# Performance work log

Hardware: AMD Instinct MI355X
Metric: run time of the kernel (lower is better)

Reference implementation:

```python
import jax, jax.numpy as jnp
import numpy as np

HID = 128
HEADS = 4
CH = HID // HEADS          # 32
EDGE_DIM = 2 * HID         # H_update mode
GROUPS = 8
NEG_SLOPE = 0.2
EPS_GN = 1e-5
EPS_LN = 1e-5
N_NODES = 32768
N_EDGES = 524288


def setup_inputs() -> dict:
    key = jax.random.key(0)
    ks = jax.random.split(key, 32)
    N, E, C = N_NODES, N_EDGES, HID
    s = lambda fan: 1.0 / np.sqrt(fan)
    inp = dict(
        h_target=jax.random.normal(ks[0], (N, C), jnp.float32),
        h_source=jax.random.normal(ks[1], (N, C), jnp.float32),
        pos=jax.random.normal(ks[2], (N, 2), jnp.float32),
        t_emb=jax.random.normal(ks[3], (N, C), jnp.float32),
        edge_index=jax.random.randint(ks[4], (2, E), 0, N, jnp.int32),
        # AdaGN params
        gn_gamma=jnp.ones((C,), jnp.float32),
        gn_beta=jnp.zeros((C,), jnp.float32),
        fc_W=jax.random.normal(ks[5], (C, 2 * C), jnp.float32) * s(C),
        fc_b=jnp.zeros((2 * C,), jnp.float32),
        # GATv2 params
        Wl=jax.random.normal(ks[6], (C, HEADS * CH), jnp.float32) * s(C),
        bl=jnp.zeros((HEADS * CH,), jnp.float32),
        Wr=jax.random.normal(ks[7], (C, HEADS * CH), jnp.float32) * s(C),
        br=jnp.zeros((HEADS * CH,), jnp.float32),
        We=jax.random.normal(ks[8], (EDGE_DIM, HEADS * CH), jnp.float32) * s(EDGE_DIM),
        att=jax.random.normal(ks[9], (HEADS, CH), jnp.float32) * s(CH),
        gat_bias=jnp.zeros((HEADS * CH,), jnp.float32),
        # post GAT linear
        Wpost=jax.random.normal(ks[10], (C, C), jnp.float32) * s(C),
        bpost=jnp.zeros((C,), jnp.float32),
        # update MLP: LayerNorm -> Linear -> GELU -> Linear
        ln_g=jnp.ones((C,), jnp.float32),
        ln_b=jnp.zeros((C,), jnp.float32),
        W1=jax.random.normal(ks[11], (C, C), jnp.float32) * s(C),
        b1=jnp.zeros((C,), jnp.float32),
        W2=jax.random.normal(ks[12], (C, C), jnp.float32) * s(C),
        b2=jnp.zeros((C,), jnp.float32),
    )
    return inp


def _adagn(x, cond, gn_gamma, gn_beta, fc_W, fc_b):
    N, C = x.shape
    xg = x.reshape(N, GROUPS, C // GROUPS)
    mu = xg.mean(-1, keepdims=True)
    var = xg.var(-1, keepdims=True)
    normed = ((xg - mu) * jax.lax.rsqrt(var + EPS_GN)).reshape(N, C)
    normed = normed * gn_gamma + gn_beta
    style = cond @ fc_W + fc_b
    gamma, beta = jnp.split(style, 2, axis=-1)
    return normed * (1.0 + gamma) + beta


def reference(h_target, h_source, pos, t_emb, edge_index,
              gn_gamma, gn_beta, fc_W, fc_b,
              Wl, bl, Wr, br, We, att, gat_bias,
              Wpost, bpost, ln_g, ln_b, W1, b1, W2, b2):
    N, C = h_source.shape
    src, dst = edge_index[0], edge_index[1]

    h_src_mod = _adagn(h_source, t_emb, gn_gamma, gn_beta, fc_W, fc_b)

    # physics edge features (H_update mode)
    d_vec = pos[src] - pos[dst]                       # [E,2]
    dx, dy = d_vec[:, 0:1], d_vec[:, 1:2]
    dist_sq = jnp.maximum((d_vec ** 2).sum(-1, keepdims=True), 1e-8)
    grad_mag = (h_src_mod[src] - h_src_mod[dst]) / dist_sq   # [E,C]
    edge_attr = jnp.concatenate([grad_mag * (-dy), grad_mag * dx], axis=-1)  # [E,2C]

    # GATv2Conv (eval mode, no dropout)
    xl = (h_src_mod @ Wl + bl).reshape(N, HEADS, CH)  # source transform
    xr = (h_src_mod @ Wr + br).reshape(N, HEADS, CH)  # target transform
    e = (edge_attr @ We).reshape(-1, HEADS, CH)
    z = jax.nn.leaky_relu(xl[src] + xr[dst] + e, NEG_SLOPE)   # [E,H,Ch]
    logit = jnp.einsum('ehc,hc->eh', z, att)                  # [E,H]
    m = jax.ops.segment_max(logit, dst, num_segments=N)       # [N,H]
    m = jnp.where(jnp.isfinite(m), m, 0.0)
    ex = jnp.exp(logit - m[dst])
    denom = jax.ops.segment_sum(ex, dst, num_segments=N)      # [N,H]
    alpha = ex / (denom[dst] + 1e-16)                         # [E,H]
    msg = xl[src] * alpha[..., None]                          # [E,H,Ch]
    aggr = jax.ops.segment_sum(msg, dst, num_segments=N).reshape(N, HEADS * CH)
    aggr = aggr + gat_bias

    aggr = aggr @ Wpost + bpost

    # update MLP with residual
    mu = aggr.mean(-1, keepdims=True)
    var = aggr.var(-1, keepdims=True)
    ln = (aggr - mu) * jax.lax.rsqrt(var + EPS_LN) * ln_g + ln_b
    h = jax.nn.gelu(ln @ W1 + b1, approximate=False) @ W2 + b2
    return h_target + h
```

## Files before the change

### kernel.cpp

```cpp
#include <hip/hip_runtime.h>
#include <hip/hip_bf16.h>
#include <math.h>

#define HID 128

typedef __bf16 bf16x8 __attribute__((ext_vector_type(8)));
typedef float f32x4 __attribute__((ext_vector_type(4)));
typedef float nf4 __attribute__((ext_vector_type(4)));
union BF8 { uint4 u; bf16x8 v; unsigned short s[8]; };

__device__ __forceinline__ unsigned short f2bf(float x) {
  unsigned u = __float_as_uint(x);
  unsigned r = u + 0x7FFFu + ((u >> 16) & 1u);
  return (unsigned short)(r >> 16);
}
__device__ __forceinline__ float bf2f(unsigned short h) {
  return __uint_as_float(((unsigned)h) << 16);
}
__device__ __forceinline__ void ld2bf(const unsigned short* p, float& x, float& y) {
  unsigned v = *(const unsigned*)p;
  x = __uint_as_float((v & 0xFFFFu) << 16);
  y = __uint_as_float(v & 0xFFFF0000u);
}
__device__ __forceinline__ float2 pk_add2(float2 a, float2 b) {
  return make_float2(a.x + b.x, a.y + b.y);
}
__device__ __forceinline__ float2 pk_sub2(float2 a, float2 b) {
  return make_float2(a.x - b.x, a.y - b.y);
}
__device__ __forceinline__ float2 pk_fma2(float2 a, float2 b, float2 c) {
  return make_float2(fmaf(a.x, b.x, c.x), fmaf(a.y, b.y, c.y));
}
__device__ __forceinline__ float2 pk_max2(float2 a, float2 b) {
  return make_float2(fmaxf(a.x, b.x), fmaxf(a.y, b.y));
}
__device__ __forceinline__ float2 pk_muls2(float2 a, float b) {
  return make_float2(a.x * b, a.y * b);
}

__global__ __launch_bounds__(256) void k1_prep_hist(
    const float* __restrict__ fc_W, const float* __restrict__ Wl,
    const float* __restrict__ Wr, const float* __restrict__ We,
    const float* __restrict__ Wpost, const float* __restrict__ W1,
    const float* __restrict__ W2, const float* __restrict__ bl,
    const float* __restrict__ br, const float* __restrict__ gat_bias,
    const float* __restrict__ bpost,
    unsigned short* __restrict__ fcTh, unsigned short* __restrict__ fcTl,
    unsigned short* __restrict__ WnTh, unsigned short* __restrict__ WnTl,
    unsigned short* __restrict__ WpT, unsigned short* __restrict__ W1T,
    unsigned short* __restrict__ W2T,
    float* __restrict__ bxy, float* __restrict__ bpost2,
    const int* __restrict__ edst, int* __restrict__ count, int E) {
  int bid = blockIdx.x;
  if (bid >= 578) {
    int e = (bid - 578) * 256 + threadIdx.x;
    if (e < E) atomicAdd(&count[edst[e]], 1);
    return;
  }
  int gid = bid * 256 + threadIdx.x;
  if (gid < 32768) {
    int n = gid >> 7, k = gid & 127;
    float x = fc_W[k * 256 + n];
    unsigned short h = f2bf(x);
    fcTh[n * 128 + k] = h;
    fcTl[n * 128 + k] = f2bf(x - bf2f(h));
  } else if (gid < 98304) {
    int i = gid - 32768; int n = i >> 7, k = i & 127;
    float x;
    if (n < 128)      x = Wl[k * 128 + n];
    else if (n < 256) x = Wr[k * 128 + (n - 128)];
    else if (n < 384) x = We[k * 128 + (n - 256)];
    else              x = We[(128 + k) * 128 + (n - 384)];
    unsigned short h = f2bf(x);
    WnTh[n * 128 + k] = h;
    if (n >= 256) WnTl[(n - 256) * 128 + k] = f2bf(x - bf2f(h));
  } else if (gid < 147456) {
    int i = gid - 98304; int which = i >> 14; int j = i & 16383;
    int n = j >> 7, k = j & 127;
    const float* W = (which == 0) ? Wpost : (which == 1) ? W1 : W2;
    unsigned short* T = (which == 0) ? WpT : (which == 1) ? W1T : W2T;
    T[n * 128 + k] = f2bf(W[k * 128 + n]);
  } else if (gid < 147712) {
    int j = gid - 147456;
    bxy[j] = (j < 128) ? bl[j] : br[j - 128];
  } else if (gid < 147840) {
    int t = gid - 147712;
    float s = bpost[t];
    for (int k = 0; k < 128; ++k) s += gat_bias[k] * Wpost[k * 128 + t];
    bpost2[t] = s;
  }
}

__global__ __launch_bounds__(256) void k2_style_scan(
    const float* __restrict__ A, const unsigned short* __restrict__ WTh,
    const unsigned short* __restrict__ WTl, const float* __restrict__ bias,
    float* __restrict__ C,
    const int* __restrict__ count, int* __restrict__ rowptr,
    int* __restrict__ cursor, int N, int E) {
  if (blockIdx.x == 512) {
    __shared__ int wtot[4];
    int t = threadIdx.x, lane = t & 63, wv = t >> 6;
    const int4* c4 = (const int4*)count;
    int base = t * 32;
    int s = 0;
    for (int i = 0; i < 32; ++i) {
      int4 c = c4[base + i];
      s += c.x + c.y + c.z + c.w;
    }
    int incl = s;
#pragma unroll
    for (int off = 1; off < 64; off <<= 1) {
      int v = __shfl_up(incl, off);
      if (lane >= off) incl += v;
    }
    if (lane == 63) wtot[wv] = incl;
    __syncthreads();
    if (t == 0) {
      int a0 = wtot[0], a1 = wtot[1], a2 = wtot[2];
      wtot[0] = 0; wtot[1] = a0; wtot[2] = a0 + a1; wtot[3] = a0 + a1 + a2;
    }
    __syncthreads();
    int run = wtot[wv] + incl - s;
    for (int i = 0; i < 32; ++i) {
      int4 c = c4[base + i];
      int4 r;
      r.x = run; run += c.x;
      r.y = run; run += c.y;
      r.z = run; run += c.z;
      r.w = run; run += c.w;
      ((int4*)rowptr)[base + i] = r;
      ((int4*)cursor)[base + i] = r;
    }
    if (t == 255) rowptr[N] = E;
    return;
  }
  int tid = threadIdx.x;
  int wave = tid >> 6, lane = tid & 63;
  int m = lane & 15, q = lane >> 4;
  int r0 = blockIdx.x * 64 + wave * 16;
  const float* arow = A + (size_t)(r0 + m) * 128 + q * 8;
  BF8 Ah[4], Al[4];
#pragma unroll
  for (int kc = 0; kc < 4; ++kc) {
    float4 x0 = *(const float4*)(arow + kc * 32);
    float4 x1 = *(const float4*)(arow + kc * 32 + 4);
    float xs[8] = {x0.x, x0.y, x0.z, x0.w, x1.x, x1.y, x1.z, x1.w};
#pragma unroll
    for (int j = 0; j < 8; ++j) {
      unsigned short h = f2bf(xs[j]);
      Ah[kc].s[j] = h;
      Al[kc].s[j] = f2bf(xs[j] - bf2f(h));
    }
  }
  for (int nt = 0; nt < 16; ++nt) {
    const unsigned short* wr  = WTh + (size_t)(nt * 16 + m) * 128 + q * 8;
    const unsigned short* wrl = WTl + (size_t)(nt * 16 + m) * 128 + q * 8;
    f32x4 acc = {0.f, 0.f, 0.f, 0.f};
#pragma unroll
    for (int kc = 0; kc < 4; ++kc) {
      BF8 bh, blo;
      bh.u  = *(const uint4*)(wr + kc * 32);
      blo.u = *(const uint4*)(wrl + kc * 32);
      acc = __builtin_amdgcn_mfma_f32_16x16x32_bf16(Ah[kc].v, bh.v, acc, 0, 0, 0);
      acc = __builtin_amdgcn_mfma_f32_16x16x32_bf16(Al[kc].v, bh.v, acc, 0, 0, 0);
      acc = __builtin_amdgcn_mfma_f32_16x16x32_bf16(Ah[kc].v, blo.v, acc, 0, 0, 0);
    }
    int n = nt * 16 + m;
    float bv = bias[n];
#pragma unroll
    for (int i = 0; i < 4; ++i) {
      int row = r0 + q * 4 + i;
      C[(size_t)row * 256 + n] = acc[i] + bv;
    }
  }
}

__global__ __launch_bounds__(256) void k3_node_scatter(
    const float* __restrict__ h_source, const float* __restrict__ style,
    const float* __restrict__ gn_gamma, const float* __restrict__ gn_beta,
    const unsigned short* __restrict__ WnTh, const unsigned short* __restrict__ WnTl,
    const float* __restrict__ bxy,
    unsigned short* __restrict__ packed, unsigned short* __restrict__ xrArr,
    const int* __restrict__ esrc, const int* __restrict__ edst,
    const float* __restrict__ pos, int* __restrict__ cursor,
    nf4* __restrict__ meta, int E) {
  int bid = blockIdx.x;
  if (bid >= 256) {
    int e = (bid - 256) * 256 + threadIdx.x;
    if (e >= E) return;
    int src = esrc[e], dst = edst[e];
    int p = atomicAdd(&cursor[dst], 1);
    float2 ps = *(const float2*)(pos + 2 * src);
    float2 pd = *(const float2*)(pos + 2 * dst);
    float dx = ps.x - pd.x, dy = ps.y - pd.y;
    float d2 = fmaxf(dx * dx + dy * dy, 1e-8f);
    nf4 v = {__int_as_float(src), -dy / d2, dx / d2, 0.0f};
    meta[p] = v;
    return;
  }
  int tid = threadIdx.x, wave = tid >> 6, lane = tid & 63;
  int m = lane & 15, q = lane >> 4;
  int r0 = bid * 128 + wave * 32;
  BF8 Ah[2][4], Al[2][4];
#pragma unroll
  for (int set = 0; set < 2; ++set) {
    int r = r0 + set * 16 + m;
    const float* hrow = h_source + (size_t)r * 128;
    const float* srow = style + (size_t)r * 256;
#pragma unroll
    for (int kc = 0; kc < 4; ++kc) {
      int ch = q * 8 + kc * 32;
      float4 x0 = *(const float4*)(hrow + ch);
      float4 x1 = *(const float4*)(hrow + ch + 4);
      float xs[8] = {x0.x, x0.y, x0.z, x0.w, x1.x, x1.y, x1.z, x1.w};
      float s8 = 0.f, q8 = 0.f;
#pragma unroll
      for (int j = 0; j < 8; ++j) { s8 += xs[j]; q8 += xs[j] * xs[j]; }
      float s16 = s8 + __shfl_xor(s8, 16);
      float q16 = q8 + __shfl_xor(q8, 16);
      float mu = s16 * (1.0f / 16.0f);
      float var = q16 * (1.0f / 16.0f) - mu * mu;
      float rv = rsqrtf(var + 1e-5f);
      float4 g0 = *(const float4*)(gn_gamma + ch);
      float4 g1 = *(const float4*)(gn_gamma + ch + 4);
      float4 be0 = *(const float4*)(gn_beta + ch);
      float4 be1 = *(const float4*)(gn_beta + ch + 4);
      float4 sg0 = *(const float4*)(srow + ch);
      float4 sg1 = *(const float4*)(srow + ch + 4);
      float4 sb0 = *(const float4*)(srow + 128 + ch);
      float4 sb1 = *(const float4*)(srow + 128 + ch + 4);
      float gg[8] = {g0.x, g0.y, g0.z, g0.w, g1.x, g1.y, g1.z, g1.w};
      float bb[8] = {be0.x, be0.y, be0.z, be0.w, be1.x, be1.y, be1.z, be1.w};
      float sg[8] = {sg0.x, sg0.y, sg0.z, sg0.w, sg1.x, sg1.y, sg1.z, sg1.w};
      float sb[8] = {sb0.x, sb0.y, sb0.z, sb0.w, sb1.x, sb1.y, sb1.z, sb1.w};
#pragma unroll
      for (int j = 0; j < 8; ++j) {
        float v = ((xs[j] - mu) * rv * gg[j] + bb[j]) * (1.0f + sg[j]) + sb[j];
        unsigned short h = f2bf(v);
        Ah[set][kc].s[j] = h;
        Al[set][kc].s[j] = f2bf(v - bf2f(h));
      }
    }
  }
  for (int nt = 0; nt < 32; ++nt) {
    f32x4 acc0 = {0.f, 0.f, 0.f, 0.f};
    f32x4 acc1 = {0.f, 0.f, 0.f, 0.f};
    const unsigned short* wr = WnTh + (size_t)(nt * 16 + m) * 128 + q * 8;
    if (nt < 16) {
#pragma unroll
      for (int kc = 0; kc < 4; ++kc) {
        BF8 bh; bh.u = *(const uint4*)(wr + kc * 32);
        acc0 = __builtin_amdgcn_mfma_f32_16x16x32_bf16(Ah[0][kc].v, bh.v, acc0, 0, 0, 0);
        acc1 = __builtin_amdgcn_mfma_f32_16x16x32_bf16(Ah[1][kc].v, bh.v, acc1, 0, 0, 0);
      }
    } else {
      const unsigned short* wl = WnTl + (size_t)((nt - 16) * 16 + m) * 128 + q * 8;
#pragma unroll
      for (int kc = 0; kc < 4; ++kc) {
        BF8 bh, blo;
        bh.u  = *(const uint4*)(wr + kc * 32);
        blo.u = *(const uint4*)(wl + kc * 32);
        acc0 = __builtin_amdgcn_mfma_f32_16x16x32_bf16(Ah[0][kc].v, bh.v, acc0, 0, 0, 0);
        acc0 = __builtin_amdgcn_mfma_f32_16x16x32_bf16(Al[0][kc].v, bh.v, acc0, 0, 0, 0);
        acc0 = __builtin_amdgcn_mfma_f32_16x16x32_bf16(Ah[0][kc].v, blo.v, acc0, 0, 0, 0);
        acc1 = __builtin_amdgcn_mfma_f32_16x16x32_bf16(Ah[1][kc].v, bh.v, acc1, 0, 0, 0);
        acc1 = __builtin_amdgcn_mfma_f32_16x16x32_bf16(Al[1][kc].v, bh.v, acc1, 0, 0, 0);
        acc1 = __builtin_amdgcn_mfma_f32_16x16x32_bf16(Ah[1][kc].v, blo.v, acc1, 0, 0, 0);
      }
    }
    int n = nt * 16 + m;
    float bv = (nt < 16) ? bxy[n] : 0.0f;
#pragma unroll
    for (int set = 0; set < 2; ++set) {
      f32x4 a = set ? acc1 : acc0;
#pragma unroll
      for (int i = 0; i < 4; ++i) {
        int row = r0 + set * 16 + q * 4 + i;
        unsigned short h = f2bf(a[i] + bv);
        if (nt < 8)       packed[(size_t)row * 384 + n] = h;
        else if (nt < 16) xrArr[(size_t)row * 128 + (n - 128)] = h;
        else              packed[(size_t)row * 384 + 128 + (n - 256)] = h;
      }
    }
  }
}

__device__ __forceinline__ void edge_step(nf4 mt, const unsigned* __restrict__ packedW,
                                          int lane, float2 xr, float2 Ad, float2 Bd,
                                          float a0, float a1,
                                          float& m, float& l, float2& s) {
  int si = __float_as_int(mt.x);
  const unsigned* pr = packedW + (size_t)si * 192;
  unsigned wxl = pr[lane];
  unsigned wA  = pr[64 + lane];
  unsigned wB  = pr[128 + lane];
  float2 xl = make_float2(__uint_as_float(wxl << 16), __uint_as_float(wxl & 0xFFFF0000u));
  float2 A  = make_float2(__uint_as_float(wA << 16),  __uint_as_float(wA & 0xFFFF0000u));
  float2 B  = make_float2(__uint_as_float(wB << 16),  __uint_as_float(wB & 0xFFFF0000u));
  float2 z = pk_add2(xl, xr);
  z = pk_fma2(make_float2(mt.y, mt.y), pk_sub2(A, Ad), z);
  z = pk_fma2(make_float2(mt.z, mt.z), pk_sub2(B, Bd), z);
  float2 zl = pk_max2(z, pk_muls2(z, 0.2f));
  float p = fmaf(a0, zl.x, a1 * zl.y);
#pragma unroll
  for (int mm = 8; mm >= 1; mm >>= 1) p += __shfl_xor(p, mm);
  if (p <= m) {
    float ex = expf(p - m);
    l += ex;
    s = pk_fma2(make_float2(ex, ex), xl, s);
  } else {
    float sc = expf(m - p);
    l = fmaf(l, sc, 1.0f);
    s = pk_fma2(make_float2(sc, sc), s, xl);
    m = p;
  }
}

__global__ __launch_bounds__(256) void k_edge(const int* __restrict__ rowptr,
                                              const nf4* __restrict__ meta,
                                              const unsigned short* __restrict__ packed,
                                              const unsigned short* __restrict__ xrArr,
                                              const float* __restrict__ att,
                                              float* __restrict__ aggr, int N) {
  int tid = threadIdx.x;
  int d = blockIdx.x * 4 + (tid >> 6);
  if (d >= N) return;
  int lane = tid & 63;
  int c0 = lane * 2;
  float2 av = *(const float2*)(att + c0);
  const unsigned* packedW = (const unsigned*)packed;
  float2 xr, Ad, Bd;
  ld2bf(xrArr + (size_t)d * 128 + c0, xr.x, xr.y);
  {
    const unsigned* pd = packedW + (size_t)d * 192;
    unsigned wA = pd[64 + lane], wB = pd[128 + lane];
    Ad = make_float2(__uint_as_float(wA << 16), __uint_as_float(wA & 0xFFFF0000u));
    Bd = make_float2(__uint_as_float(wB << 16), __uint_as_float(wB & 0xFFFF0000u));
  }
  int beg = rowptr[d], end = rowptr[d + 1];
  float m1 = -INFINITY, l1 = 0.f; float2 s1 = make_float2(0.f, 0.f);
  float m2 = -INFINITY, l2 = 0.f; float2 s2 = make_float2(0.f, 0.f);
  int j = beg;
  if (j + 1 < end) {
    nf4 mt0 = meta[j], mt1 = meta[j + 1];
    for (; j + 3 < end; j += 2) {
      nf4 nx0 = meta[j + 2], nx1 = meta[j + 3];
      edge_step(mt0, packedW, lane, xr, Ad, Bd, av.x, av.y, m1, l1, s1);
      edge_step(mt1, packedW, lane, xr, Ad, Bd, av.x, av.y, m2, l2, s2);
      mt0 = nx0; mt1 = nx1;
    }
    edge_step(mt0, packedW, lane, xr, Ad, Bd, av.x, av.y, m1, l1, s1);
    edge_step(mt1, packedW, lane, xr, Ad, Bd, av.x, av.y, m2, l2, s2);
    j += 2;
  }
  if (j < end) {
    nf4 mt = meta[j];
    edge_step(mt, packedW, lane, xr, Ad, Bd, av.x, av.y, m1, l1, s1);
  }
  float nm = fmaxf(m1, m2);
  float sc1 = (m1 == nm) ? 1.0f : expf(m1 - nm);
  float sc2 = (m2 == nm) ? 1.0f : expf(m2 - nm);
  float l = fmaf(l1, sc1, l2 * sc2);
  float o0 = fmaf(s1.x, sc1, s2.x * sc2);
  float o1 = fmaf(s1.y, sc1, s2.y * sc2);
  float inv = 1.0f / (l + 1e-16f);
  *(float2*)&aggr[(size_t)d * 128 + c0] = make_float2(o0 * inv, o1 * inv);
}

__global__ __launch_bounds__(256) void k_mlp(const float* __restrict__ aggr,
                                             const unsigned short* __restrict__ WpT,
                                             const unsigned short* __restrict__ W1T,
                                             const unsigned short* __restrict__ W2T,
                                             const float* __restrict__ bpost2,
                                             const float* __restrict__ b1,
                                             const float* __restrict__ b2,
                                             const float* __restrict__ ln_g,
                                             const float* __restrict__ ln_b,
                                             const float* __restrict__ h_target,
                                             float* __restrict__ out) {
  __shared__ unsigned short Tb[64 * 136];
  __shared__ unsigned short Ub[64 * 136];
  int tid = threadIdx.x, wave = tid >> 6, lane = tid & 63;
  int m = lane & 15, q = lane >> 4;
  int r0 = blockIdx.x * 64 + wave * 16;
  int rb0 = wave * 16;
  BF8 Af[4];
  {
    const float* arow = aggr + (size_t)(r0 + m) * 128 + q * 8;
#pragma unroll
    for (int kc = 0; kc < 4; ++kc) {
      float4 x0 = *(const float4*)(arow + kc * 32);
      float4 x1 = *(const float4*)(arow + kc * 32 + 4);
      float xs[8] = {x0.x, x0.y, x0.z, x0.w, x1.x, x1.y, x1.z, x1.w};
#pragma unroll
      for (int jj = 0; jj < 8; ++jj) Af[kc].s[jj] = f2bf(xs[jj]);
    }
  }
  f32x4 acc[8];
#pragma unroll
  for (int t = 0; t < 8; ++t) {
    const unsigned short* wr = WpT + (size_t)(t * 16 + m) * 128 + q * 8;
    f32x4 a = {0.f, 0.f, 0.f, 0.f};
#pragma unroll
    for (int kc = 0; kc < 4; ++kc) {
      BF8 bh; bh.u = *(const uint4*)(wr + kc * 32);
      a = __builtin_amdgcn_mfma_f32_16x16x32_bf16(Af[kc].v, bh.v, a, 0, 0, 0);
    }
    acc[t] = a;
  }
  float sum[4] = {0, 0, 0, 0}, sq[4] = {0, 0, 0, 0};
#pragma unroll
  for (int t = 0; t < 8; ++t) {
    float bv = bpost2[t * 16 + m];
#pragma unroll
    for (int i = 0; i < 4; ++i) {
      float v = acc[t][i] + bv;
      acc[t][i] = v;
      sum[i] += v;
      sq[i] += v * v;
    }
  }
#pragma unroll
  for (int i = 0; i < 4; ++i) {
#pragma unroll
    for (int w = 1; w <= 8; w <<= 1) {
      sum[i] += __shfl_xor(sum[i], w);
      sq[i] += __shfl_xor(sq[i], w);
    }
  }
  float mu[4], rv[4];
#pragma unroll
  for (int i = 0; i < 4; ++i) {
    mu[i] = sum[i] * (1.0f / 128.0f);
    float var = sq[i] * (1.0f / 128.0f) - mu[i] * mu[i];
    rv[i] = rsqrtf(var + 1e-5f);
  }
#pragma unroll
  for (int t = 0; t < 8; ++t) {
    int n = t * 16 + m;
    float g = ln_g[n], b = ln_b[n];
#pragma unroll
    for (int i = 0; i < 4; ++i) {
      float v = (acc[t][i] - mu[i]) * rv[i] * g + b;
      Tb[(rb0 + q * 4 + i) * 136 + n] = f2bf(v);
    }
  }
  __syncthreads();
  BF8 Bf[4];
  {
    const unsigned short* tp = Tb + (rb0 + m) * 136 + q * 8;
#pragma unroll
    for (int kc = 0; kc < 4; ++kc) Bf[kc].u = *(const uint4*)(tp + kc * 32);
  }
#pragma unroll
  for (int t = 0; t < 8; ++t) {
    const unsigned short* wr = W1T + (size_t)(t * 16 + m) * 128 + q * 8;
    f32x4 a = {0.f, 0.f, 0.f, 0.f};
#pragma unroll
    for (int kc = 0; kc < 4; ++kc) {
      BF8 bh; bh.u = *(const uint4*)(wr + kc * 32);
      a = __builtin_amdgcn_mfma_f32_16x16x32_bf16(Bf[kc].v, bh.v, a, 0, 0, 0);
    }
    acc[t] = a;
  }
#pragma unroll
  for (int t = 0; t < 8; ++t) {
    int n = t * 16 + m;
    float bv = b1[n];
#pragma unroll
    for (int i = 0; i < 4; ++i) {
      float v = acc[t][i] + bv;
      v = 0.5f * v * (1.0f + erff(v * 0.70710678118654752f));
      Ub[(rb0 + q * 4 + i) * 136 + n] = f2bf(v);
    }
  }
  __syncthreads();
  BF8 Cf[4];
  {
    const unsigned short* up = Ub + (rb0 + m) * 136 + q * 8;
#pragma unroll
    for (int kc = 0; kc < 4; ++kc) Cf[kc].u = *(const uint4*)(up + kc * 32);
  }
#pragma unroll
  for (int t = 0; t < 8; ++t) {
    const unsigned short* wr = W2T + (size_t)(t * 16 + m) * 128 + q * 8;
    f32x4 a = {0.f, 0.f, 0.f, 0.f};
#pragma unroll
    for (int kc = 0; kc < 4; ++kc) {
      BF8 bh; bh.u = *(const uint4*)(wr + kc * 32);
      a = __builtin_amdgcn_mfma_f32_16x16x32_bf16(Cf[kc].v, bh.v, a, 0, 0, 0);
    }
    int n = t * 16 + m;
    float bv = b2[n];
#pragma unroll
    for (int i = 0; i < 4; ++i) {
      size_t off = (size_t)(r0 + q * 4 + i) * 128 + n;
      out[off] = a[i] + bv + h_target[off];
    }
  }
}

extern "C" void kernel_launch(void* const* d_in, const int* in_sizes, int n_in,
                              void* d_out, int out_size, void* d_ws, size_t ws_size,
                              hipStream_t stream) {
  const float* h_target = (const float*)d_in[0];
  const float* h_source = (const float*)d_in[1];
  const float* pos      = (const float*)d_in[2];
  const float* t_emb    = (const float*)d_in[3];
  const int*   eidx     = (const int*)d_in[4];
  const float* gn_gamma = (const float*)d_in[5];
  const float* gn_beta  = (const float*)d_in[6];
  const float* fc_W     = (const float*)d_in[7];
  const float* fc_b     = (const float*)d_in[8];
  const float* Wl       = (const float*)d_in[9];
  const float* bl       = (const float*)d_in[10];
  const float* Wr       = (const float*)d_in[11];
  const float* br       = (const float*)d_in[12];
  const float* We       = (const float*)d_in[13];
  const float* att      = (const float*)d_in[14];
  const float* gat_bias = (const float*)d_in[15];
  const float* Wpost    = (const float*)d_in[16];
  const float* bpost    = (const float*)d_in[17];
  const float* ln_g     = (const float*)d_in[18];
  const float* ln_b     = (const float*)d_in[19];
  const float* W1       = (const float*)d_in[20];
  const float* b1       = (const float*)d_in[21];
  const float* W2       = (const float*)d_in[22];
  const float* b2       = (const float*)d_in[23];

  const int N = in_sizes[0] / HID;
  const int E = in_sizes[4] / 2;
  const int* esrc = eidx;
  const int* edst = eidx + E;

  float* ws = (float*)d_ws;
  const size_t MF = 1024 * 1024;
  float* style  = ws;
  float* aggr   = ws;
  unsigned short* packed = (unsigned short*)(ws + 8 * MF);
  unsigned short* xrArr  = (unsigned short*)(ws + 14 * MF);
  nf4*   meta   = (nf4*)(ws + 16 * MF);
  int*   rowptr = (int*)(ws + 18 * MF);
  int*   count  = rowptr + 32832;
  int*   cursor = count + 32832;
  unsigned short* wgt = (unsigned short*)(ws + 18 * MF + 131072);
  unsigned short* fcTh = wgt;
  unsigned short* fcTl = wgt + 32768;
  unsigned short* WnTh = wgt + 65536;
  unsigned short* WnTl = wgt + 131072;
  unsigned short* WpT  = wgt + 163840;
  unsigned short* W1T  = wgt + 180224;
  unsigned short* W2T  = wgt + 196608;
  float* bxy    = (float*)(wgt + 212992);
  float* bpost2 = bxy + 256;
  const size_t needed = (size_t)(18 * MF + 131072 + 106496 + 512) * 4;
  if (ws_size < needed) return;

  dim3 blk(256);
  const int histB = (E + 255) / 256;

  (void)hipMemsetAsync(count, 0, (size_t)N * 4, stream);
  k1_prep_hist<<<578 + histB, blk, 0, stream>>>(
      fc_W, Wl, Wr, We, Wpost, W1, W2, bl, br, gat_bias, bpost,
      fcTh, fcTl, WnTh, WnTl, WpT, W1T, W2T, bxy, bpost2, edst, count, E);
  k2_style_scan<<<513, blk, 0, stream>>>(t_emb, fcTh, fcTl, fc_b, style,
                                         count, rowptr, cursor, N, E);
  k3_node_scatter<<<256 + histB, blk, 0, stream>>>(
      h_source, style, gn_gamma, gn_beta, WnTh, WnTl, bxy, packed, xrArr,
      esrc, edst, pos, cursor, meta, E);
  k_edge<<<(N + 3) / 4, blk, 0, stream>>>(rowptr, meta, packed, xrArr, att, aggr, N);
  k_mlp<<<N / 64, blk, 0, stream>>>(aggr, WpT, W1T, W2T, bpost2, b1, b2, ln_g, ln_b,
                                    h_target, (float*)d_out);
}
```

Baseline: 363.5 us.

## Interleave packed node features, store aggr in bf16, reshuffle kernel pipeline

```diff
diff --git a/kernel.cpp b/kernel.cpp
--- a/kernel.cpp
+++ b/kernel.cpp
@@ -8,6 +8,7 @@
 typedef float f32x4 __attribute__((ext_vector_type(4)));
 typedef float nf4 __attribute__((ext_vector_type(4)));
 union BF8 { uint4 u; bf16x8 v; unsigned short s[8]; };
+struct U3 { unsigned x, y, z; };
 
 __device__ __forceinline__ unsigned short f2bf(float x) {
   unsigned u = __float_as_uint(x);
@@ -22,6 +23,9 @@
   x = __uint_as_float((v & 0xFFFFu) << 16);
   y = __uint_as_float(v & 0xFFFF0000u);
 }
+__device__ __forceinline__ float2 unpk(unsigned w) {
+  return make_float2(__uint_as_float(w << 16), __uint_as_float(w & 0xFFFF0000u));
+}
 __device__ __forceinline__ float2 pk_add2(float2 a, float2 b) {
   return make_float2(a.x + b.x, a.y + b.y);
 }
@@ -38,7 +42,7 @@
   return make_float2(a.x * b, a.y * b);
 }
 
-__global__ __launch_bounds__(256) void k1_prep_hist(
+__global__ __launch_bounds__(256) void k1_prep_zero(
     const float* __restrict__ fc_W, const float* __restrict__ Wl,
     const float* __restrict__ Wr, const float* __restrict__ We,
     const float* __restrict__ Wpost, const float* __restrict__ W1,
@@ -50,11 +54,11 @@
     unsigned short* __restrict__ WpT, unsigned short* __restrict__ W1T,
     unsigned short* __restrict__ W2T,
     float* __restrict__ bxy, float* __restrict__ bpost2,
-    const int* __restrict__ edst, int* __restrict__ count, int E) {
+    int* __restrict__ count) {
   int bid = blockIdx.x;
   if (bid >= 578) {
-    int e = (bid - 578) * 256 + threadIdx.x;
-    if (e < E) atomicAdd(&count[edst[e]], 1);
+    int i = (bid - 578) * 256 + threadIdx.x;
+    ((int4*)count)[i] = make_int4(0, 0, 0, 0);
     return;
   }
   int gid = bid * 256 + threadIdx.x;
@@ -91,13 +95,66 @@
   }
 }
 
-__global__ __launch_bounds__(256) void k2_style_scan(
+__global__ __launch_bounds__(256) void k2_style_hist(
     const float* __restrict__ A, const unsigned short* __restrict__ WTh,
     const unsigned short* __restrict__ WTl, const float* __restrict__ bias,
     float* __restrict__ C,
+    const int* __restrict__ edst, int* __restrict__ count, int E) {
+  if (blockIdx.x >= 512) {
+    int e = (blockIdx.x - 512) * 256 + threadIdx.x;
+    if (e < E) atomicAdd(&count[edst[e]], 1);
+    return;
+  }
+  int tid = threadIdx.x;
+  int wave = tid >> 6, lane = tid & 63;
+  int m = lane & 15, q = lane >> 4;
+  int r0 = blockIdx.x * 64 + wave * 16;
+  const float* arow = A + (size_t)(r0 + m) * 128 + q * 8;
+  BF8 Ah[4], Al[4];
+#pragma unroll
+  for (int kc = 0; kc < 4; ++kc) {
+    float4 x0 = *(const float4*)(arow + kc * 32);
+    float4 x1 = *(const float4*)(arow + kc * 32 + 4);
+    float xs[8] = {x0.x, x0.y, x0.z, x0.w, x1.x, x1.y, x1.z, x1.w};
+#pragma unroll
+    for (int j = 0; j < 8; ++j) {
+      unsigned short h = f2bf(xs[j]);
+      Ah[kc].s[j] = h;
+      Al[kc].s[j] = f2bf(xs[j] - bf2f(h));
+    }
+  }
+  for (int nt = 0; nt < 16; ++nt) {
+    const unsigned short* wr  = WTh + (size_t)(nt * 16 + m) * 128 + q * 8;
+    const unsigned short* wrl = WTl + (size_t)(nt * 16 + m) * 128 + q * 8;
+    f32x4 acc = {0.f, 0.f, 0.f, 0.f};
+#pragma unroll
+    for (int kc = 0; kc < 4; ++kc) {
+      BF8 bh, blo;
+      bh.u  = *(const uint4*)(wr + kc * 32);
+      blo.u = *(const uint4*)(wrl + kc * 32);
+      acc = __builtin_amdgcn_mfma_f32_16x16x32_bf16(Ah[kc].v, bh.v, acc, 0, 0, 0);
+      acc = __builtin_amdgcn_mfma_f32_16x16x32_bf16(Al[kc].v, bh.v, acc, 0, 0, 0);
+      acc = __builtin_amdgcn_mfma_f32_16x16x32_bf16(Ah[kc].v, blo.v, acc, 0, 0, 0);
+    }
+    int n = nt * 16 + m;
+    float bv = bias[n];
+#pragma unroll
+    for (int i = 0; i < 4; ++i) {
+      int row = r0 + q * 4 + i;
+      C[(size_t)row * 256 + n] = acc[i] + bv;
+    }
+  }
+}
+
+__global__ __launch_bounds__(256) void k3_node_scan(
+    const float* __restrict__ h_source, const float* __restrict__ style,
+    const float* __restrict__ gn_gamma, const float* __restrict__ gn_beta,
+    const unsigned short* __restrict__ WnTh, const unsigned short* __restrict__ WnTl,
+    const float* __restrict__ bxy,
+    unsigned short* __restrict__ packed, unsigned short* __restrict__ xrArr,
     const int* __restrict__ count, int* __restrict__ rowptr,
     int* __restrict__ cursor, int N, int E) {
-  if (blockIdx.x == 512) {
+  if (blockIdx.x == 256) {
     __shared__ int wtot[4];
     int t = threadIdx.x, lane = t & 63, wv = t >> 6;
     const int4* c4 = (const int4*)count;
@@ -134,73 +191,9 @@
     if (t == 255) rowptr[N] = E;
     return;
   }
-  int tid = threadIdx.x;
-  int wave = tid >> 6, lane = tid & 63;
-  int m = lane & 15, q = lane >> 4;
-  int r0 = blockIdx.x * 64 + wave * 16;
-  const float* arow = A + (size_t)(r0 + m) * 128 + q * 8;
-  BF8 Ah[4], Al[4];
-#pragma unroll
-  for (int kc = 0; kc < 4; ++kc) {
-    float4 x0 = *(const float4*)(arow + kc * 32);
-    float4 x1 = *(const float4*)(arow + kc * 32 + 4);
-    float xs[8] = {x0.x, x0.y, x0.z, x0.w, x1.x, x1.y, x1.z, x1.w};
-#pragma unroll
-    for (int j = 0; j < 8; ++j) {
-      unsigned short h = f2bf(xs[j]);
-      Ah[kc].s[j] = h;
-      Al[kc].s[j] = f2bf(xs[j] - bf2f(h));
-    }
-  }
-  for (int nt = 0; nt < 16; ++nt) {
-    const unsigned short* wr  = WTh + (size_t)(nt * 16 + m) * 128 + q * 8;
-    const unsigned short* wrl = WTl + (size_t)(nt * 16 + m) * 128 + q * 8;
-    f32x4 acc = {0.f, 0.f, 0.f, 0.f};
-#pragma unroll
-    for (int kc = 0; kc < 4; ++kc) {
-      BF8 bh, blo;
-      bh.u  = *(const uint4*)(wr + kc * 32);
-      blo.u = *(const uint4*)(wrl + kc * 32);
-      acc = __builtin_amdgcn_mfma_f32_16x16x32_bf16(Ah[kc].v, bh.v, acc, 0, 0, 0);
-      acc = __builtin_amdgcn_mfma_f32_16x16x32_bf16(Al[kc].v, bh.v, acc, 0, 0, 0);
-      acc = __builtin_amdgcn_mfma_f32_16x16x32_bf16(Ah[kc].v, blo.v, acc, 0, 0, 0);
-    }
-    int n = nt * 16 + m;
-    float bv = bias[n];
-#pragma unroll
-    for (int i = 0; i < 4; ++i) {
-      int row = r0 + q * 4 + i;
-      C[(size_t)row * 256 + n] = acc[i] + bv;
-    }
-  }
-}
-
-__global__ __launch_bounds__(256) void k3_node_scatter(
-    const float* __restrict__ h_source, const float* __restrict__ style,
-    const float* __restrict__ gn_gamma, const float* __restrict__ gn_beta,
-    const unsigned short* __restrict__ WnTh, const unsigned short* __restrict__ WnTl,
-    const float* __restrict__ bxy,
-    unsigned short* __restrict__ packed, unsigned short* __restrict__ xrArr,
-    const int* __restrict__ esrc, const int* __restrict__ edst,
-    const float* __restrict__ pos, int* __restrict__ cursor,
-    nf4* __restrict__ meta, int E) {
-  int bid = blockIdx.x;
-  if (bid >= 256) {
-    int e = (bid - 256) * 256 + threadIdx.x;
-    if (e >= E) return;
-    int src = esrc[e], dst = edst[e];
-    int p = atomicAdd(&cursor[dst], 1);
-    float2 ps = *(const float2*)(pos + 2 * src);
-    float2 pd = *(const float2*)(pos + 2 * dst);
-    float dx = ps.x - pd.x, dy = ps.y - pd.y;
-    float d2 = fmaxf(dx * dx + dy * dy, 1e-8f);
-    nf4 v = {__int_as_float(src), -dy / d2, dx / d2, 0.0f};
-    meta[p] = v;
-    return;
-  }
   int tid = threadIdx.x, wave = tid >> 6, lane = tid & 63;
   int m = lane & 15, q = lane >> 4;
-  int r0 = bid * 128 + wave * 32;
+  int r0 = blockIdx.x * 128 + wave * 32;
   BF8 Ah[2][4], Al[2][4];
 #pragma unroll
   for (int set = 0; set < 2; ++set) {
@@ -277,26 +270,42 @@
       for (int i = 0; i < 4; ++i) {
         int row = r0 + set * 16 + q * 4 + i;
         unsigned short h = f2bf(a[i] + bv);
-        if (nt < 8)       packed[(size_t)row * 384 + n] = h;
+        size_t pb = (size_t)row * 384;
+        if (nt < 8)       packed[pb + (n >> 1) * 6 + (n & 1)] = h;
         else if (nt < 16) xrArr[(size_t)row * 128 + (n - 128)] = h;
-        else              packed[(size_t)row * 384 + 128 + (n - 256)] = h;
+        else if (nt < 24) { int c = n - 256; packed[pb + (c >> 1) * 6 + 2 + (c & 1)] = h; }
+        else              { int c = n - 384; packed[pb + (c >> 1) * 6 + 4 + (c & 1)] = h; }
       }
     }
   }
 }
 
-__device__ __forceinline__ void edge_step(nf4 mt, const unsigned* __restrict__ packedW,
+__global__ __launch_bounds__(256) void k_scatter(const int* __restrict__ esrc,
+                                                 const int* __restrict__ edst,
+                                                 const float* __restrict__ pos,
+                                                 int* __restrict__ cursor,
+                                                 nf4* __restrict__ meta, int E) {
+  int e = blockIdx.x * 256 + threadIdx.x;
+  if (e >= E) return;
+  int src = esrc[e], dst = edst[e];
+  int p = atomicAdd(&cursor[dst], 1);
+  float2 ps = *(const float2*)(pos + 2 * src);
+  float2 pd = *(const float2*)(pos + 2 * dst);
+  float dx = ps.x - pd.x, dy = ps.y - pd.y;
+  float d2 = fmaxf(dx * dx + dy * dy, 1e-8f);
+  nf4 v = {__int_as_float(src), -dy / d2, dx / d2, 0.0f};
+  meta[p] = v;
+}
+
+__device__ __forceinline__ void edge_step(nf4 mt, const U3* __restrict__ packed3,
                                           int lane, float2 xr, float2 Ad, float2 Bd,
                                           float a0, float a1,
                                           float& m, float& l, float2& s) {
   int si = __float_as_int(mt.x);
-  const unsigned* pr = packedW + (size_t)si * 192;
-  unsigned wxl = pr[lane];
-  unsigned wA  = pr[64 + lane];
-  unsigned wB  = pr[128 + lane];
-  float2 xl = make_float2(__uint_as_float(wxl << 16), __uint_as_float(wxl & 0xFFFF0000u));
-  float2 A  = make_float2(__uint_as_float(wA << 16),  __uint_as_float(wA & 0xFFFF0000u));
-  float2 B  = make_float2(__uint_as_float(wB << 16),  __uint_as_float(wB & 0xFFFF0000u));
+  U3 w = packed3[(size_t)si * 64 + lane];
+  float2 xl = unpk(w.x);
+  float2 A  = unpk(w.y);
+  float2 B  = unpk(w.z);
   float2 z = pk_add2(xl, xr);
   z = pk_fma2(make_float2(mt.y, mt.y), pk_sub2(A, Ad), z);
   z = pk_fma2(make_float2(mt.z, mt.z), pk_sub2(B, Bd), z);
@@ -305,11 +314,11 @@
 #pragma unroll
   for (int mm = 8; mm >= 1; mm >>= 1) p += __shfl_xor(p, mm);
   if (p <= m) {
-    float ex = expf(p - m);
+    float ex = __expf(p - m);
     l += ex;
     s = pk_fma2(make_float2(ex, ex), xl, s);
   } else {
-    float sc = expf(m - p);
+    float sc = __expf(m - p);
     l = fmaf(l, sc, 1.0f);
     s = pk_fma2(make_float2(sc, sc), s, xl);
     m = p;
@@ -321,21 +330,20 @@
                                               const unsigned short* __restrict__ packed,
                                               const unsigned short* __restrict__ xrArr,
                                               const float* __restrict__ att,
-                                              float* __restrict__ aggr, int N) {
+                                              unsigned* __restrict__ aggr16, int N) {
   int tid = threadIdx.x;
   int d = blockIdx.x * 4 + (tid >> 6);
   if (d >= N) return;
   int lane = tid & 63;
   int c0 = lane * 2;
   float2 av = *(const float2*)(att + c0);
-  const unsigned* packedW = (const unsigned*)packed;
+  const U3* packed3 = (const U3*)packed;
   float2 xr, Ad, Bd;
   ld2bf(xrArr + (size_t)d * 128 + c0, xr.x, xr.y);
   {
-    const unsigned* pd = packedW + (size_t)d * 192;
-    unsigned wA = pd[64 + lane], wB = pd[128 + lane];
-    Ad = make_float2(__uint_as_float(wA << 16), __uint_as_float(wA & 0xFFFF0000u));
-    Bd = make_float2(__uint_as_float(wB << 16), __uint_as_float(wB & 0xFFFF0000u));
+    U3 wd = packed3[(size_t)d * 64 + lane];
+    Ad = unpk(wd.y);
+    Bd = unpk(wd.z);
   }
   int beg = rowptr[d], end = rowptr[d + 1];
   float m1 = -INFINITY, l1 = 0.f; float2 s1 = make_float2(0.f, 0.f);
@@ -345,29 +353,29 @@
     nf4 mt0 = meta[j], mt1 = meta[j + 1];
     for (; j + 3 < end; j += 2) {
       nf4 nx0 = meta[j + 2], nx1 = meta[j + 3];
-      edge_step(mt0, packedW, lane, xr, Ad, Bd, av.x, av.y, m1, l1, s1);
-      edge_step(mt1, packedW, lane, xr, Ad, Bd, av.x, av.y, m2, l2, s2);
+      edge_step(mt0, packed3, lane, xr, Ad, Bd, av.x, av.y, m1, l1, s1);
+      edge_step(mt1, packed3, lane, xr, Ad, Bd, av.x, av.y, m2, l2, s2);
       mt0 = nx0; mt1 = nx1;
     }
-    edge_step(mt0, packedW, lane, xr, Ad, Bd, av.x, av.y, m1, l1, s1);
-    edge_step(mt1, packedW, lane, xr, Ad, Bd, av.x, av.y, m2, l2, s2);
+    edge_step(mt0, packed3, lane, xr, Ad, Bd, av.x, av.y, m1, l1, s1);
+    edge_step(mt1, packed3, lane, xr, Ad, Bd, av.x, av.y, m2, l2, s2);
     j += 2;
   }
   if (j < end) {
     nf4 mt = meta[j];
-    edge_step(mt, packedW, lane, xr, Ad, Bd, av.x, av.y, m1, l1, s1);
+    edge_step(mt, packed3, lane, xr, Ad, Bd, av.x, av.y, m1, l1, s1);
   }
   float nm = fmaxf(m1, m2);
-  float sc1 = (m1 == nm) ? 1.0f : expf(m1 - nm);
-  float sc2 = (m2 == nm) ? 1.0f : expf(m2 - nm);
+  float sc1 = (m1 == nm) ? 1.0f : __expf(m1 - nm);
+  float sc2 = (m2 == nm) ? 1.0f : __expf(m2 - nm);
   float l = fmaf(l1, sc1, l2 * sc2);
   float o0 = fmaf(s1.x, sc1, s2.x * sc2);
   float o1 = fmaf(s1.y, sc1, s2.y * sc2);
   float inv = 1.0f / (l + 1e-16f);
-  *(float2*)&aggr[(size_t)d * 128 + c0] = make_float2(o0 * inv, o1 * inv);
-}
-
-__global__ __launch_bounds__(256) void k_mlp(const float* __restrict__ aggr,
+  aggr16[(size_t)d * 64 + lane] = (unsigned)f2bf(o0 * inv) | ((unsigned)f2bf(o1 * inv) << 16);
+}
+
+__global__ __launch_bounds__(256) void k_mlp(const unsigned short* __restrict__ aggr16,
                                              const unsigned short* __restrict__ WpT,
                                              const unsigned short* __restrict__ W1T,
                                              const unsigned short* __restrict__ W2T,
@@ -386,15 +394,9 @@
   int rb0 = wave * 16;
   BF8 Af[4];
   {
-    const float* arow = aggr + (size_t)(r0 + m) * 128 + q * 8;
-#pragma unroll
-    for (int kc = 0; kc < 4; ++kc) {
-      float4 x0 = *(const float4*)(arow + kc * 32);
-      float4 x1 = *(const float4*)(arow + kc * 32 + 4);
-      float xs[8] = {x0.x, x0.y, x0.z, x0.w, x1.x, x1.y, x1.z, x1.w};
-#pragma unroll
-      for (int jj = 0; jj < 8; ++jj) Af[kc].s[jj] = f2bf(xs[jj]);
-    }
+    const unsigned short* arow = aggr16 + (size_t)(r0 + m) * 128 + q * 8;
+#pragma unroll
+    for (int kc = 0; kc < 4; ++kc) Af[kc].u = *(const uint4*)(arow + kc * 32);
   }
   f32x4 acc[8];
 #pragma unroll
@@ -536,7 +538,7 @@
   float* ws = (float*)d_ws;
   const size_t MF = 1024 * 1024;
   float* style  = ws;
-  float* aggr   = ws;
+  unsigned* aggr16 = (unsigned*)ws;
   unsigned short* packed = (unsigned short*)(ws + 8 * MF);
   unsigned short* xrArr  = (unsigned short*)(ws + 14 * MF);
   nf4*   meta   = (nf4*)(ws + 16 * MF);
@@ -559,16 +561,15 @@
   dim3 blk(256);
   const int histB = (E + 255) / 256;
 
-  (void)hipMemsetAsync(count, 0, (size_t)N * 4, stream);
-  k1_prep_hist<<<578 + histB, blk, 0, stream>>>(
+  k1_prep_zero<<<610, blk, 0, stream>>>(
       fc_W, Wl, Wr, We, Wpost, W1, W2, bl, br, gat_bias, bpost,
-      fcTh, fcTl, WnTh, WnTl, WpT, W1T, W2T, bxy, bpost2, edst, count, E);
-  k2_style_scan<<<513, blk, 0, stream>>>(t_emb, fcTh, fcTl, fc_b, style,
-                                         count, rowptr, cursor, N, E);
-  k3_node_scatter<<<256 + histB, blk, 0, stream>>>(
-      h_source, style, gn_gamma, gn_beta, WnTh, WnTl, bxy, packed, xrArr,
-      esrc, edst, pos, cursor, meta, E);
-  k_edge<<<(N + 3) / 4, blk, 0, stream>>>(rowptr, meta, packed, xrArr, att, aggr, N);
-  k_mlp<<<N / 64, blk, 0, stream>>>(aggr, WpT, W1T, W2T, bpost2, b1, b2, ln_g, ln_b,
-                                    h_target, (float*)d_out);
-}
+      fcTh, fcTl, WnTh, WnTl, WpT, W1T, W2T, bxy, bpost2, count);
+  k2_style_hist<<<512 + histB, blk, 0, stream>>>(t_emb, fcTh, fcTl, fc_b, style,
+                                                 edst, count, E);
+  k3_node_scan<<<257, blk, 0, stream>>>(h_source, style, gn_gamma, gn_beta, WnTh, WnTl,
+                                        bxy, packed, xrArr, count, rowptr, cursor, N, E);
+  k_scatter<<<histB, blk, 0, stream>>>(esrc, edst, pos, cursor, meta, E);
+  k_edge<<<(N + 3) / 4, blk, 0, stream>>>(rowptr, meta, packed, xrArr, att, aggr16, N);
+  k_mlp<<<N / 64, blk, 0, stream>>>((const unsigned short*)aggr16, WpT, W1T, W2T, bpost2,
+                                    b1, b2, ln_g, ln_b, h_target, (float*)d_out);
+}
```

New measurement: 364.1 us. About the same (+0.1%).
